# Performance work log

Measured on AMD Instinct MI355X. Metric: run time of the kernel, lower is better.

The kernel has to match this reference:

```python
import jax, jax.numpy as jnp
from jax import lax
import numpy as np

# dims
N_DIA, DLEN = 48, 64            # 48 dialogues, 64 utterances each
N = N_DIA * DLEN                # total utterances = 3072
D = 512                         # n_dim (modal feature dim)
H = 512                         # nhidden
NL = 2                          # GCNII layers
NS = 2                          # n_speakers
ALPHA, LAMDA = 0.1, 0.5
PI = float(np.pi)
SCALE = 0.99999                 # acos clamp factor from original code


def setup_inputs() -> dict:
    key = jax.random.key(0)
    ks = jax.random.split(key, 8)
    a = jax.random.normal(ks[0], (N, D), jnp.float32)
    v = jax.random.normal(ks[1], (N, D), jnp.float32)
    l = jax.random.normal(ks[2], (N, D), jnp.float32)
    qmask = jax.random.uniform(ks[3], (DLEN, N_DIA, NS), jnp.float32)
    dia_len = np.full((N_DIA,), DLEN, dtype=np.int64)  # static segment lengths
    # learned params
    W_spk = 0.02 * jax.random.normal(ks[4], (NS, D), jnp.float32)      # speaker_embeddings
    W0 = jax.random.normal(ks[5], (D, H), jnp.float32) / np.sqrt(D)    # graph_net.fcs[0]
    b0 = jnp.zeros((H,), jnp.float32)
    Wg = jax.random.normal(ks[6], (NL, H, H), jnp.float32) / np.sqrt(H)  # GCNII conv weights
    return {"a": a, "v": v, "l": l, "qmask": qmask, "dia_len": dia_len,
            "W_spk": W_spk, "W0": W0, "b0": b0, "Wg": Wg}


def _angular_sim(cs):
    # 1 - acos(cs*0.99999)/pi, clipped for numerical safety of acos
    return 1.0 - jnp.arccos(jnp.clip(cs * SCALE, -SCALE, SCALE)) / PI


def _build_adj(feats, seg_mask):
    # feats: list of 3 arrays [N, D]; seg_mask: [N, N] same-dialogue block mask
    n = feats[0].shape[0]
    normed = [f * jax.lax.rsqrt(jnp.sum(f * f, axis=1, keepdims=True)) for f in feats]
    adj = jnp.zeros((3 * n, 3 * n), feats[0].dtype)
    ar = jnp.arange(n)
    for m in range(3):
        for nn_ in range(3):
            if m == nn_:
                # within-modality: block-diagonal (per dialogue) angular cosine similarity
                sim = _angular_sim(normed[m] @ normed[m].T) * seg_mask
                adj = adj.at[m * n:(m + 1) * n, nn_ * n:(nn_ + 1) * n].set(sim)
            else:
                # cross-modality: only diagonal (same utterance) entries
                cs = jnp.sum(normed[m] * normed[nn_], axis=1)
                adj = adj.at[m * n + ar, nn_ * n + ar].set(_angular_sim(cs))
    # symmetric degree normalization D^-1/2 A D^-1/2
    dinv = jax.lax.rsqrt(adj.sum(axis=1))
    return adj * dinv[:, None] * dinv[None, :]


def reference(a, v, l, qmask, dia_len, W_spk, W0, b0, Wg):
    dl = np.asarray(dia_len)
    nb = dl.shape[0]
    # node -> (position-in-dialogue, dialogue-id), static from dia_len
    dia_id = np.repeat(np.arange(nb), dl)
    pos = np.concatenate([np.arange(x) for x in dl])
    qflat = qmask[pos, dia_id]                 # [N, NS], matches torch.cat order
    spk_idx = jnp.argmax(qflat, axis=-1)       # [N]
    l = l + W_spk[spk_idx]                     # use_speaker=True, 'l' in modals

    seg = jnp.asarray(dia_id)
    seg_mask = (seg[:, None] == seg[None, :]).astype(a.dtype)  # [N, N]
    adj = _build_adj([a, v, l], seg_mask)      # [3N, 3N]

    x = jnp.concatenate([a, v, l], axis=0)     # [3N, D]
    # GCNII_lyc (eval mode: dropout is identity)
    h0 = jax.nn.relu(x @ W0 + b0)              # [3N, H]
    thetas = jnp.log(LAMDA / jnp.arange(1, NL + 1, dtype=x.dtype) + 1.0)

    def step(h, wt):
        W, theta = wt
        hi = adj @ h
        support = (1.0 - ALPHA) * hi + ALPHA * h0   # variant=False
        h = jax.nn.relu(theta * (support @ W) + (1.0 - theta) * support)
        return h, None

    h, _ = lax.scan(step, h0, (Wg, thetas))
    feat = jnp.concatenate([x, h], axis=-1)    # use_residue=True -> [3N, D+H]
    n = a.shape[0]
    # regroup per-utterance modal features: [N, 3*(D+H)]
    out = jnp.concatenate([feat[:n], feat[n:2 * n], feat[2 * n:3 * n]], axis=-1)
    return out
```

## Files before the change

### kernel.cpp

```cpp
#include <hip/hip_runtime.h>
#include <math.h>

#define N_DIA 48
#define NTOT  3072
#define DD    512
#define M3    9216
#define SEG   ((size_t)NTOT * DD)

#define SCALE_F 0.99999f
#define PI_F    3.14159274101257324f

typedef __attribute__((ext_vector_type(8))) short frag8;
typedef __attribute__((ext_vector_type(4))) float f32x4;

__device__ __forceinline__ float ang_sim(float cs) {
    float cc = cs * SCALE_F;
    cc = fminf(fmaxf(cc, -SCALE_F), SCALE_F);
    return 1.0f - acosf(cc) / PI_F;
}
__device__ __forceinline__ unsigned short f2bf(float x) {
    union { float f; unsigned int u; } c; c.f = x;
    unsigned int r = c.u + 0x7fffu + ((c.u >> 16) & 1u);
    return (unsigned short)(r >> 16);
}
__device__ __forceinline__ float bf2f(unsigned short h) {
    union { unsigned int u; float f; } c; c.u = ((unsigned int)h) << 16;
    return c.f;
}
__device__ __forceinline__ void gload16(const unsigned short* g, unsigned short* s) {
    __builtin_amdgcn_global_load_lds(
        (const __attribute__((address_space(1))) unsigned int*)g,
        (__attribute__((address_space(3))) unsigned int*)s, 16, 0, 0);
}

__global__ __launch_bounds__(64) void k_pre(
    const float* __restrict__ a, const float* __restrict__ v,
    const float* __restrict__ l, const float* __restrict__ qmask,
    const float* __restrict__ Wspk,
    float* __restrict__ out, unsigned short* __restrict__ xb,
    float* __restrict__ invn, float* __restrict__ cross)
{
    int i = blockIdx.x, t = threadIdx.x;
    int pos = i & 63, dia = i >> 6;
    int qb = (pos * N_DIA + dia) * 2;
    float q0 = qmask[qb], q1 = qmask[qb + 1];
    int spk = (q0 >= q1) ? 0 : 1;
    const float4* av4 = (const float4*)(a + (size_t)i * DD);
    const float4* vv4 = (const float4*)(v + (size_t)i * DD);
    const float4* lv4 = (const float4*)(l + (size_t)i * DD);
    const float4* wv4 = (const float4*)(Wspk + (size_t)spk * DD);
    float* ob = out + (size_t)i * 3072;
    float saa = 0, svv = 0, sll = 0, sav = 0, sal = 0, svl = 0;
#pragma unroll
    for (int e = 0; e < 2; e++) {
        int idx = t * 2 + e;
        float4 xa = av4[idx], xv = vv4[idx], xd = lv4[idx], xw = wv4[idx];
        float4 xL = make_float4(xd.x + xw.x, xd.y + xw.y, xd.z + xw.z, xd.w + xw.w);
        *(float4*)(ob + idx * 4)        = xa;
        *(float4*)(ob + 1024 + idx * 4) = xv;
        *(float4*)(ob + 2048 + idx * 4) = xL;
        ushort4 ya, yv, yl;
        ya.x = f2bf(xa.x); ya.y = f2bf(xa.y); ya.z = f2bf(xa.z); ya.w = f2bf(xa.w);
        yv.x = f2bf(xv.x); yv.y = f2bf(xv.y); yv.z = f2bf(xv.z); yv.w = f2bf(xv.w);
        yl.x = f2bf(xL.x); yl.y = f2bf(xL.y); yl.z = f2bf(xL.z); yl.w = f2bf(xL.w);
        *(ushort4*)(xb + (size_t)i * DD + idx * 4) = ya;
        *(ushort4*)(xb + SEG + (size_t)i * DD + idx * 4) = yv;
        *(ushort4*)(xb + 2 * SEG + (size_t)i * DD + idx * 4) = yl;
        saa += xa.x * xa.x + xa.y * xa.y + xa.z * xa.z + xa.w * xa.w;
        svv += xv.x * xv.x + xv.y * xv.y + xv.z * xv.z + xv.w * xv.w;
        sll += xL.x * xL.x + xL.y * xL.y + xL.z * xL.z + xL.w * xL.w;
        sav += xa.x * xv.x + xa.y * xv.y + xa.z * xv.z + xa.w * xv.w;
        sal += xa.x * xL.x + xa.y * xL.y + xa.z * xL.z + xa.w * xL.w;
        svl += xv.x * xL.x + xv.y * xL.y + xv.z * xL.z + xv.w * xL.w;
    }
#pragma unroll
    for (int off = 32; off; off >>= 1) {
        saa += __shfl_down(saa, off, 64);
        svv += __shfl_down(svv, off, 64);
        sll += __shfl_down(sll, off, 64);
        sav += __shfl_down(sav, off, 64);
        sal += __shfl_down(sal, off, 64);
        svl += __shfl_down(svl, off, 64);
    }
    if (t == 0) {
        float ina = 1.0f / sqrtf(saa);
        float inv_ = 1.0f / sqrtf(svv);
        float inl = 1.0f / sqrtf(sll);
        invn[i] = ina; invn[NTOT + i] = inv_; invn[2 * NTOT + i] = inl;
        cross[i]            = ang_sim(sav * ina * inv_);
        cross[NTOT + i]     = ang_sim(sal * ina * inl);
        cross[2 * NTOT + i] = ang_sim(svl * inv_ * inl);
    }
}

__global__ __launch_bounds__(256) void k_gram_mfma(
    const unsigned short* __restrict__ xb, const float* __restrict__ invn,
    const float* __restrict__ cross, float* __restrict__ blk,
    float* __restrict__ dinv)
{
    __shared__ __align__(16) unsigned short Xs[16 * 2048];
    int d = blockIdx.x, m = blockIdx.y;
    int t = threadIdx.x;
    int lane = t & 63, wv = t >> 6;
    int mrow = m * NTOT + d * 64;
    const unsigned short* src = xb + (size_t)mrow * DD;
#pragma unroll
    for (int c = 0; c < 16; c++) {
        gload16(src + (size_t)(t >> 2) * DD + c * 32 + (t & 3) * 8,
                &Xs[c * 2048 + wv * 512]);
    }
    __syncthreads();

    int rsel = lane & 15, quad = lane >> 4;
    f32x4 acc[4];
#pragma unroll
    for (int j = 0; j < 4; j++) acc[j] = (f32x4){0.f, 0.f, 0.f, 0.f};
#pragma unroll
    for (int c = 0; c < 16; c++) {
        const unsigned short* base = &Xs[c * 2048];
        frag8 bf[4];
#pragma unroll
        for (int j = 0; j < 4; j++)
            bf[j] = *(const frag8*)&base[(j * 16 + rsel) * 32 + quad * 8];
        frag8 af = *(const frag8*)&base[(wv * 16 + rsel) * 32 + quad * 8];
#pragma unroll
        for (int j = 0; j < 4; j++)
            acc[j] = __builtin_amdgcn_mfma_f32_16x16x32_bf16(af, bf[j], acc[j], 0, 0, 0);
    }

    size_t bbase = (size_t)(m * N_DIA + d) * 4096;
    int rowl0 = wv * 16 + quad * 4;
    float ir[4], rs[4] = {0.f, 0.f, 0.f, 0.f};
#pragma unroll
    for (int r = 0; r < 4; r++) ir[r] = invn[mrow + rowl0 + r];
#pragma unroll
    for (int j = 0; j < 4; j++) {
        int coll = j * 16 + rsel;
        float ic = invn[mrow + coll];
#pragma unroll
        for (int r = 0; r < 4; r++) {
            float sim = ang_sim(acc[j][r] * ir[r] * ic);
            blk[bbase + (size_t)(rowl0 + r) * 64 + coll] = sim;
            rs[r] += sim;
        }
    }
#pragma unroll
    for (int off = 8; off; off >>= 1)
#pragma unroll
        for (int r = 0; r < 4; r++) rs[r] += __shfl_down(rs[r], off, 16);
    if (rsel == 0) {
#pragma unroll
        for (int r = 0; r < 4; r++) {
            int gi = d * 64 + rowl0 + r;
            float c1, c2;
            if (m == 0)      { c1 = cross[gi];        c2 = cross[NTOT + gi]; }
            else if (m == 1) { c1 = cross[gi];        c2 = cross[2 * NTOT + gi]; }
            else             { c1 = cross[NTOT + gi]; c2 = cross[2 * NTOT + gi]; }
            dinv[m * NTOT + gi] = 1.0f / sqrtf(rs[r] + c1 + c2);
        }
    }
}

__global__ void k_wt(const float* __restrict__ W0, const float* __restrict__ Wg,
                     unsigned short* __restrict__ Wt) {
    __shared__ float tile[32][33];
    int bx = blockIdx.x, by = blockIdx.y, mm = blockIdx.z;
    const float* W = (mm == 0) ? W0 : Wg + (size_t)(mm - 1) * DD * DD;
    int t = threadIdx.x;
    int tx = t & 31, ty = t >> 5;
#pragma unroll
    for (int q = 0; q < 4; q++) {
        int k = by * 32 + ty + q * 8;
        tile[ty + q * 8][tx] = W[(size_t)k * DD + bx * 32 + tx];
    }
    __syncthreads();
#pragma unroll
    for (int q = 0; q < 4; q++) {
        int n = bx * 32 + ty + q * 8;
        Wt[(size_t)mm * DD * DD + (size_t)n * DD + by * 32 + tx] = f2bf(tile[tx][ty + q * 8]);
    }
}

__global__ __launch_bounds__(256) void k_gemm_mfma(
    const unsigned short* __restrict__ A, const unsigned short* __restrict__ Wt,
    const float* __restrict__ bias, const unsigned short* __restrict__ resid,
    unsigned short* __restrict__ outT, unsigned short* __restrict__ outR,
    float* __restrict__ outF, float theta, int mode)
{
    __shared__ __align__(16) unsigned short As[64 * 32];
    __shared__ __align__(16) unsigned short Bs[128 * 32];
    int t = threadIdx.x;
    int lane = t & 63, wv = t >> 6;
    int mbase = blockIdx.y * 64, nbase = blockIdx.x * 128;
    int srow = lane >> 2;
    int scol = (lane & 3) * 8;
    int rsel = lane & 15, quad = lane >> 4;

    const unsigned short* Ag  = A  + (size_t)(mbase + wv * 16 + srow) * DD + scol;
    const unsigned short* Bg0 = Wt + (size_t)(nbase + wv * 32 + srow) * DD + scol;
    const unsigned short* Bg1 = Wt + (size_t)(nbase + wv * 32 + 16 + srow) * DD + scol;
    unsigned short* Asl  = &As[wv * 512];
    unsigned short* Bsl0 = &Bs[wv * 1024];
    unsigned short* Bsl1 = &Bs[wv * 1024 + 512];

    f32x4 acc[8];
#pragma unroll
    for (int i = 0; i < 8; i++) acc[i] = (f32x4){0.f, 0.f, 0.f, 0.f};

    for (int kt = 0; kt < DD; kt += 32) {
        __syncthreads();
        gload16(Ag + kt, Asl);
        gload16(Bg0 + kt, Bsl0);
        gload16(Bg1 + kt, Bsl1);
        __syncthreads();
        frag8 af[4], bfr[2];
#pragma unroll
        for (int i = 0; i < 4; i++)
            af[i] = *(const frag8*)&As[(i * 16 + rsel) * 32 + quad * 8];
#pragma unroll
        for (int j = 0; j < 2; j++)
            bfr[j] = *(const frag8*)&Bs[(wv * 32 + j * 16 + rsel) * 32 + quad * 8];
#pragma unroll
        for (int i = 0; i < 4; i++)
#pragma unroll
            for (int j = 0; j < 2; j++)
                acc[i * 2 + j] = __builtin_amdgcn_mfma_f32_16x16x32_bf16(
                    af[i], bfr[j], acc[i * 2 + j], 0, 0, 0);
    }

    float omt = 1.0f - theta;
    int mq = mbase / NTOT;
    int iu0 = mbase - mq * NTOT;
#pragma unroll
    for (int i = 0; i < 4; i++)
#pragma unroll
        for (int j = 0; j < 2; j++) {
            int col = nbase + wv * 32 + j * 16 + rsel;
            int rowl = i * 16 + quad * 4;
            int rowb = mbase + rowl;
            f32x4 r = acc[i * 2 + j];
            float vv[4];
#pragma unroll
            for (int rr = 0; rr < 4; rr++) {
                float x = r[rr];
                if (mode == 0) x += bias[col];
                else x = theta * x + omt * bf2f(resid[(size_t)(rowb + rr) * DD + col]);
                vv[rr] = fmaxf(x, 0.f);
            }
            if (mode == 2) {
#pragma unroll
                for (int rr = 0; rr < 4; rr++)
                    outF[(size_t)(iu0 + rowl + rr) * 3072 + mq * 1024 + 512 + col] = vv[rr];
            } else {
                ushort4 w4;
                w4.x = f2bf(vv[0]); w4.y = f2bf(vv[1]);
                w4.z = f2bf(vv[2]); w4.w = f2bf(vv[3]);
                *(ushort4*)(outT + (size_t)col * M3 + rowb) = w4;
#pragma unroll
                for (int rr = 0; rr < 4; rr++)
                    outR[(size_t)(rowb + rr) * DD + col] = f2bf(vv[rr]);
            }
        }
}

__global__ __launch_bounds__(256) void k_adjmul_mfma(
    const float* __restrict__ blk, const float* __restrict__ cross,
    const float* __restrict__ dinv,
    const unsigned short* __restrict__ hT, const unsigned short* __restrict__ hrow,
    const unsigned short* __restrict__ h0row, unsigned short* __restrict__ supb)
{
    __shared__ __align__(16) unsigned short AdL[64 * 72];
    __shared__ __align__(16) unsigned short hTL[256 * 72];
    __shared__ float dv[64];
    int cc = blockIdx.x, d = blockIdx.y, m = blockIdx.z;
    int t = threadIdx.x;
    int lane = t & 63, wv = t >> 6;
    int dbase = d * 64, cbase = cc * 256;
    int rsel = lane & 15, quad = lane >> 4;

    if (t < 64) dv[t] = dinv[m * NTOT + dbase + t];
    __syncthreads();

    size_t bbase = (size_t)(m * N_DIA + d) * 4096;
#pragma unroll
    for (int q = 0; q < 4; q++) {
        int e4 = t + 256 * q;
        int i = e4 >> 4, j4 = e4 & 15;
        float4 w = *(const float4*)(blk + bbase + (size_t)i * 64 + j4 * 4);
        float di = dv[i];
        ushort4 o;
        o.x = f2bf(w.x * di * dv[j4 * 4 + 0]);
        o.y = f2bf(w.y * di * dv[j4 * 4 + 1]);
        o.z = f2bf(w.z * di * dv[j4 * 4 + 2]);
        o.w = f2bf(w.w * di * dv[j4 * 4 + 3]);
        *(ushort4*)&AdL[i * 72 + j4 * 4] = o;
    }
#pragma unroll
    for (int p = 0; p < 8; p++) {
        int e = t + 256 * p;
        int cl = e >> 3;
        int jo = (e & 7) * 8;
        uint4 w = *(const uint4*)(hT + (size_t)(cbase + cl) * M3 + m * NTOT + dbase + jo);
        *(uint4*)&hTL[cl * 72 + jo] = w;
    }
    __syncthreads();

    f32x4 acc[16];
#pragma unroll
    for (int i = 0; i < 16; i++) acc[i] = (f32x4){0.f, 0.f, 0.f, 0.f};
#pragma unroll
    for (int kk = 0; kk < 2; kk++) {
        frag8 bfr[4];
#pragma unroll
        for (int it = 0; it < 4; it++)
            bfr[it] = *(const frag8*)&AdL[(it * 16 + rsel) * 72 + kk * 32 + quad * 8];
#pragma unroll
        for (int jc = 0; jc < 4; jc++) {
            frag8 af = *(const frag8*)&hTL[(wv * 64 + jc * 16 + rsel) * 72 + kk * 32 + quad * 8];
#pragma unroll
            for (int it = 0; it < 4; it++)
                acc[jc * 4 + it] = __builtin_amdgcn_mfma_f32_16x16x32_bf16(
                    af, bfr[it], acc[jc * 4 + it], 0, 0, 0);
        }
    }

    int n1, n2, p1, p2;
    if (m == 0)      { n1 = 1; n2 = 2; p1 = 0; p2 = 1; }
    else if (m == 1) { n1 = 0; n2 = 2; p1 = 0; p2 = 2; }
    else             { n1 = 0; n2 = 1; p1 = 1; p2 = 2; }
#pragma unroll
    for (int it = 0; it < 4; it++) {
        int il = it * 16 + rsel;
        int gi = dbase + il;
        float dm = dv[il];
        float cv1 = cross[p1 * NTOT + gi] * dm * dinv[n1 * NTOT + gi];
        float cv2 = cross[p2 * NTOT + gi] * dm * dinv[n2 * NTOT + gi];
        size_t r1 = (size_t)(n1 * NTOT + gi) * DD;
        size_t r2 = (size_t)(n2 * NTOT + gi) * DD;
        size_t r0 = (size_t)(m * NTOT + gi) * DD;
#pragma unroll
        for (int jc = 0; jc < 4; jc++) {
            int cb = cbase + wv * 64 + jc * 16 + quad * 4;
            ushort4 u1 = *(const ushort4*)(hrow + r1 + cb);
            ushort4 u2 = *(const ushort4*)(hrow + r2 + cb);
            ushort4 u0 = *(const ushort4*)(h0row + r0 + cb);
            f32x4 aa = acc[jc * 4 + it];
            ushort4 w;
            w.x = f2bf(0.9f * (aa[0] + cv1 * bf2f(u1.x) + cv2 * bf2f(u2.x)) + 0.1f * bf2f(u0.x));
            w.y = f2bf(0.9f * (aa[1] + cv1 * bf2f(u1.y) + cv2 * bf2f(u2.y)) + 0.1f * bf2f(u0.y));
            w.z = f2bf(0.9f * (aa[2] + cv1 * bf2f(u1.z) + cv2 * bf2f(u2.z)) + 0.1f * bf2f(u0.z));
            w.w = f2bf(0.9f * (aa[3] + cv1 * bf2f(u1.w) + cv2 * bf2f(u2.w)) + 0.1f * bf2f(u0.w));
            *(ushort4*)(supb + r0 + cb) = w;
        }
    }
}

extern "C" void kernel_launch(void* const* d_in, const int* in_sizes, int n_in,
                              void* d_out, int out_size, void* d_ws, size_t ws_size,
                              hipStream_t stream) {
    (void)in_sizes; (void)n_in; (void)out_size; (void)ws_size;
    const float* a     = (const float*)d_in[0];
    const float* v     = (const float*)d_in[1];
    const float* l     = (const float*)d_in[2];
    const float* qmask = (const float*)d_in[3];
    const float* Wspk  = (const float*)d_in[5];
    const float* W0    = (const float*)d_in[6];
    const float* b0    = (const float*)d_in[7];
    const float* Wg    = (const float*)d_in[8];
    float* out = (float*)d_out;
    float* ws = (float*)d_ws;

    float* invn  = ws;
    float* blk   = invn + M3;
    float* cross = blk + (size_t)3 * N_DIA * 4096;
    float* dinvp = cross + M3;
    unsigned short* Wt  = (unsigned short*)(dinvp + M3);
    unsigned short* xb  = Wt + (size_t)3 * DD * DD;
    unsigned short* supb = xb;
    unsigned short* h0T = xb + 3 * SEG;
    unsigned short* h0r = h0T + 3 * SEG;
    unsigned short* h1T = h0r + 3 * SEG;
    unsigned short* h1r = h1T + 3 * SEG;

    k_pre<<<NTOT, 64, 0, stream>>>(a, v, l, qmask, Wspk, out, xb, invn, cross);
    k_wt <<<dim3(16, 16, 3), 256, 0, stream>>>(W0, Wg, Wt);
    k_gram_mfma<<<dim3(N_DIA, 3), 256, 0, stream>>>(xb, invn, cross, blk, dinvp);

    const float th1 = 0.40546510810816438f;
    const float th2 = 0.22314355131420976f;

    k_gemm_mfma<<<dim3(4, 144), 256, 0, stream>>>(xb, Wt, b0, nullptr,
                                                  h0T, h0r, nullptr, 0.f, 0);
    k_adjmul_mfma<<<dim3(2, N_DIA, 3), 256, 0, stream>>>(blk, cross, dinvp,
                                                         h0T, h0r, h0r, supb);
    k_gemm_mfma<<<dim3(4, 144), 256, 0, stream>>>(supb, Wt + (size_t)DD * DD, nullptr, supb,
                                                  h1T, h1r, nullptr, th1, 1);
    k_adjmul_mfma<<<dim3(2, N_DIA, 3), 256, 0, stream>>>(blk, cross, dinvp,
                                                         h1T, h1r, h0r, supb);
    k_gemm_mfma<<<dim3(4, 144), 256, 0, stream>>>(supb, Wt + (size_t)2 * DD * DD, nullptr, supb,
                                                  nullptr, nullptr, out, th2, 2);
}
```

Measured before the change: 204.2 us.

## Reassociate GCNII layers to apply weights before adjacency, fuse prep kernels, swizzle LDS

Reorders each GCNII layer so the feature transform (theta*W + (1-theta)I) is applied before the adjacency multiply, which is valid because that map is linear. The adjacency kernel then emits the final ReLU output directly. This also removes a separate output GEMM pass, and the second layer's h0 transform is batched into the same GEMM launch. The prep and weight-transpose kernels are merged into one launch, and the GEMM gets double-buffered LDS loads with XOR-swizzled layouts. Outputs are staged through LDS for coalesced stores, and LDS bank conflicts are reduced in the gram and adjacency kernels. The reordering changes where bf16 rounding happens, which shifts numerics slightly.

```diff
diff --git a/kernel.cpp b/kernel.cpp
--- a/kernel.cpp
+++ b/kernel.cpp
@@ -33,63 +33,87 @@
         (__attribute__((address_space(3))) unsigned int*)s, 16, 0, 0);
 }
 
-__global__ __launch_bounds__(64) void k_pre(
+__global__ __launch_bounds__(256) void k_pre_wt(
     const float* __restrict__ a, const float* __restrict__ v,
     const float* __restrict__ l, const float* __restrict__ qmask,
-    const float* __restrict__ Wspk,
+    const float* __restrict__ Wspk, const float* __restrict__ W0,
+    const float* __restrict__ Wg,
     float* __restrict__ out, unsigned short* __restrict__ xb,
-    float* __restrict__ invn, float* __restrict__ cross)
+    float* __restrict__ invn, float* __restrict__ cross,
+    unsigned short* __restrict__ Wt)
 {
-    int i = blockIdx.x, t = threadIdx.x;
-    int pos = i & 63, dia = i >> 6;
-    int qb = (pos * N_DIA + dia) * 2;
-    float q0 = qmask[qb], q1 = qmask[qb + 1];
-    int spk = (q0 >= q1) ? 0 : 1;
-    const float4* av4 = (const float4*)(a + (size_t)i * DD);
-    const float4* vv4 = (const float4*)(v + (size_t)i * DD);
-    const float4* lv4 = (const float4*)(l + (size_t)i * DD);
-    const float4* wv4 = (const float4*)(Wspk + (size_t)spk * DD);
-    float* ob = out + (size_t)i * 3072;
-    float saa = 0, svv = 0, sll = 0, sav = 0, sal = 0, svl = 0;
-#pragma unroll
-    for (int e = 0; e < 2; e++) {
-        int idx = t * 2 + e;
-        float4 xa = av4[idx], xv = vv4[idx], xd = lv4[idx], xw = wv4[idx];
-        float4 xL = make_float4(xd.x + xw.x, xd.y + xw.y, xd.z + xw.z, xd.w + xw.w);
-        *(float4*)(ob + idx * 4)        = xa;
-        *(float4*)(ob + 1024 + idx * 4) = xv;
-        *(float4*)(ob + 2048 + idx * 4) = xL;
-        ushort4 ya, yv, yl;
-        ya.x = f2bf(xa.x); ya.y = f2bf(xa.y); ya.z = f2bf(xa.z); ya.w = f2bf(xa.w);
-        yv.x = f2bf(xv.x); yv.y = f2bf(xv.y); yv.z = f2bf(xv.z); yv.w = f2bf(xv.w);
-        yl.x = f2bf(xL.x); yl.y = f2bf(xL.y); yl.z = f2bf(xL.z); yl.w = f2bf(xL.w);
-        *(ushort4*)(xb + (size_t)i * DD + idx * 4) = ya;
-        *(ushort4*)(xb + SEG + (size_t)i * DD + idx * 4) = yv;
-        *(ushort4*)(xb + 2 * SEG + (size_t)i * DD + idx * 4) = yl;
-        saa += xa.x * xa.x + xa.y * xa.y + xa.z * xa.z + xa.w * xa.w;
-        svv += xv.x * xv.x + xv.y * xv.y + xv.z * xv.z + xv.w * xv.w;
-        sll += xL.x * xL.x + xL.y * xL.y + xL.z * xL.z + xL.w * xL.w;
-        sav += xa.x * xv.x + xa.y * xv.y + xa.z * xv.z + xa.w * xv.w;
-        sal += xa.x * xL.x + xa.y * xL.y + xa.z * xL.z + xa.w * xL.w;
-        svl += xv.x * xL.x + xv.y * xL.y + xv.z * xL.z + xv.w * xL.w;
-    }
-#pragma unroll
-    for (int off = 32; off; off >>= 1) {
-        saa += __shfl_down(saa, off, 64);
-        svv += __shfl_down(svv, off, 64);
-        sll += __shfl_down(sll, off, 64);
-        sav += __shfl_down(sav, off, 64);
-        sal += __shfl_down(sal, off, 64);
-        svl += __shfl_down(svl, off, 64);
-    }
-    if (t == 0) {
-        float ina = 1.0f / sqrtf(saa);
-        float inv_ = 1.0f / sqrtf(svv);
-        float inl = 1.0f / sqrtf(sll);
-        invn[i] = ina; invn[NTOT + i] = inv_; invn[2 * NTOT + i] = inl;
-        cross[i]            = ang_sim(sav * ina * inv_);
-        cross[NTOT + i]     = ang_sim(sal * ina * inl);
-        cross[2 * NTOT + i] = ang_sim(svl * inv_ * inl);
+    __shared__ float tile[32][33];
+    int b = blockIdx.x;
+    if (b < 768) {
+        int wv = threadIdx.x >> 6, t = threadIdx.x & 63;
+        int i = b * 4 + wv;
+        int pos = i & 63, dia = i >> 6;
+        int qb = (pos * N_DIA + dia) * 2;
+        float q0 = qmask[qb], q1 = qmask[qb + 1];
+        int spk = (q0 >= q1) ? 0 : 1;
+        const float4* av4 = (const float4*)(a + (size_t)i * DD);
+        const float4* vv4 = (const float4*)(v + (size_t)i * DD);
+        const float4* lv4 = (const float4*)(l + (size_t)i * DD);
+        const float4* wv4 = (const float4*)(Wspk + (size_t)spk * DD);
+        float* ob = out + (size_t)i * 3072;
+        float saa = 0, svv = 0, sll = 0, sav = 0, sal = 0, svl = 0;
+#pragma unroll
+        for (int e = 0; e < 2; e++) {
+            int idx = t * 2 + e;
+            float4 xa = av4[idx], xv = vv4[idx], xd = lv4[idx], xw = wv4[idx];
+            float4 xL = make_float4(xd.x + xw.x, xd.y + xw.y, xd.z + xw.z, xd.w + xw.w);
+            *(float4*)(ob + idx * 4)        = xa;
+            *(float4*)(ob + 1024 + idx * 4) = xv;
+            *(float4*)(ob + 2048 + idx * 4) = xL;
+            ushort4 ya, yv, yl;
+            ya.x = f2bf(xa.x); ya.y = f2bf(xa.y); ya.z = f2bf(xa.z); ya.w = f2bf(xa.w);
+            yv.x = f2bf(xv.x); yv.y = f2bf(xv.y); yv.z = f2bf(xv.z); yv.w = f2bf(xv.w);
+            yl.x = f2bf(xL.x); yl.y = f2bf(xL.y); yl.z = f2bf(xL.z); yl.w = f2bf(xL.w);
+            *(ushort4*)(xb + (size_t)i * DD + idx * 4) = ya;
+            *(ushort4*)(xb + SEG + (size_t)i * DD + idx * 4) = yv;
+            *(ushort4*)(xb + 2 * SEG + (size_t)i * DD + idx * 4) = yl;
+            saa += xa.x * xa.x + xa.y * xa.y + xa.z * xa.z + xa.w * xa.w;
+            svv += xv.x * xv.x + xv.y * xv.y + xv.z * xv.z + xv.w * xv.w;
+            sll += xL.x * xL.x + xL.y * xL.y + xL.z * xL.z + xL.w * xL.w;
+            sav += xa.x * xv.x + xa.y * xv.y + xa.z * xv.z + xa.w * xv.w;
+            sal += xa.x * xL.x + xa.y * xL.y + xa.z * xL.z + xa.w * xL.w;
+            svl += xv.x * xL.x + xv.y * xL.y + xv.z * xL.z + xv.w * xL.w;
+        }
+#pragma unroll
+        for (int off = 32; off; off >>= 1) {
+            saa += __shfl_down(saa, off, 64);
+            svv += __shfl_down(svv, off, 64);
+            sll += __shfl_down(sll, off, 64);
+            sav += __shfl_down(sav, off, 64);
+            sal += __shfl_down(sal, off, 64);
+            svl += __shfl_down(svl, off, 64);
+        }
+        if (t == 0) {
+            float ina = 1.0f / sqrtf(saa);
+            float inv_ = 1.0f / sqrtf(svv);
+            float inl = 1.0f / sqrtf(sll);
+            invn[i] = ina; invn[NTOT + i] = inv_; invn[2 * NTOT + i] = inl;
+            cross[i]            = ang_sim(sav * ina * inv_);
+            cross[NTOT + i]     = ang_sim(sal * ina * inl);
+            cross[2 * NTOT + i] = ang_sim(svl * inv_ * inl);
+        }
+    } else {
+        int idx = b - 768;
+        int mm = idx >> 8;
+        int by = (idx >> 4) & 15, bx = idx & 15;
+        const float* W = (mm == 0) ? W0 : Wg + (size_t)(mm - 1) * DD * DD;
+        int t = threadIdx.x, tx = t & 31, ty = t >> 5;
+#pragma unroll
+        for (int q = 0; q < 4; q++) {
+            int k = by * 32 + ty + q * 8;
+            tile[ty + q * 8][tx] = W[(size_t)k * DD + bx * 32 + tx];
+        }
+        __syncthreads();
+#pragma unroll
+        for (int q = 0; q < 4; q++) {
+            int n = bx * 32 + ty + q * 8;
+            Wt[(size_t)mm * DD * DD + (size_t)n * DD + by * 32 + tx] = f2bf(tile[tx][ty + q * 8]);
+        }
     }
 }
 
@@ -104,14 +128,16 @@
     int lane = t & 63, wv = t >> 6;
     int mrow = m * NTOT + d * 64;
     const unsigned short* src = xb + (size_t)mrow * DD;
+    int sunit = ((t & 3) ^ ((t >> 2) & 3)) * 8;
 #pragma unroll
     for (int c = 0; c < 16; c++) {
-        gload16(src + (size_t)(t >> 2) * DD + c * 32 + (t & 3) * 8,
+        gload16(src + (size_t)(t >> 2) * DD + c * 32 + sunit,
                 &Xs[c * 2048 + wv * 512]);
     }
     __syncthreads();
 
     int rsel = lane & 15, quad = lane >> 4;
+    int sq = (quad ^ (rsel & 3)) * 8;
     f32x4 acc[4];
 #pragma unroll
     for (int j = 0; j < 4; j++) acc[j] = (f32x4){0.f, 0.f, 0.f, 0.f};
@@ -121,8 +147,8 @@
         frag8 bf[4];
 #pragma unroll
         for (int j = 0; j < 4; j++)
-            bf[j] = *(const frag8*)&base[(j * 16 + rsel) * 32 + quad * 8];
-        frag8 af = *(const frag8*)&base[(wv * 16 + rsel) * 32 + quad * 8];
+            bf[j] = *(const frag8*)&base[(j * 16 + rsel) * 32 + sq];
+        frag8 af = *(const frag8*)&base[(wv * 16 + rsel) * 32 + sq];
 #pragma unroll
         for (int j = 0; j < 4; j++)
             acc[j] = __builtin_amdgcn_mfma_f32_16x16x32_bf16(af, bf[j], acc[j], 0, 0, 0);
@@ -161,65 +187,65 @@
     }
 }
 
-__global__ void k_wt(const float* __restrict__ W0, const float* __restrict__ Wg,
-                     unsigned short* __restrict__ Wt) {
-    __shared__ float tile[32][33];
-    int bx = blockIdx.x, by = blockIdx.y, mm = blockIdx.z;
-    const float* W = (mm == 0) ? W0 : Wg + (size_t)(mm - 1) * DD * DD;
-    int t = threadIdx.x;
-    int tx = t & 31, ty = t >> 5;
-#pragma unroll
-    for (int q = 0; q < 4; q++) {
-        int k = by * 32 + ty + q * 8;
-        tile[ty + q * 8][tx] = W[(size_t)k * DD + bx * 32 + tx];
-    }
-    __syncthreads();
-#pragma unroll
-    for (int q = 0; q < 4; q++) {
-        int n = bx * 32 + ty + q * 8;
-        Wt[(size_t)mm * DD * DD + (size_t)n * DD + by * 32 + tx] = f2bf(tile[tx][ty + q * 8]);
-    }
-}
-
-__global__ __launch_bounds__(256) void k_gemm_mfma(
-    const unsigned short* __restrict__ A, const unsigned short* __restrict__ Wt,
-    const float* __restrict__ bias, const unsigned short* __restrict__ resid,
-    unsigned short* __restrict__ outT, unsigned short* __restrict__ outR,
-    float* __restrict__ outF, float theta, int mode)
+__global__ __launch_bounds__(256) void k_gemm(
+    const unsigned short* __restrict__ A, const unsigned short* __restrict__ W,
+    const float* __restrict__ bias,
+    unsigned short* __restrict__ oRows, unsigned short* __restrict__ oT,
+    float theta, int mode,
+    const unsigned short* __restrict__ A2, unsigned short* __restrict__ oRows2)
 {
-    __shared__ __align__(16) unsigned short As[64 * 32];
-    __shared__ __align__(16) unsigned short Bs[128 * 32];
-    int t = threadIdx.x;
-    int lane = t & 63, wv = t >> 6;
-    int mbase = blockIdx.y * 64, nbase = blockIdx.x * 128;
+    __shared__ __align__(16) char smem[53248];
+    unsigned short* const As0 = (unsigned short*)smem;
+    unsigned short* const As1 = (unsigned short*)(smem + 4096);
+    unsigned short* const Bs0 = (unsigned short*)(smem + 8192);
+    unsigned short* const Bs1 = (unsigned short*)(smem + 16384);
+    unsigned short* const tH  = (unsigned short*)smem;
+    unsigned short* const tR  = (unsigned short*)(smem + 17408);
+    unsigned short* const tT  = (unsigned short*)(smem + 34816);
+
+    int t = threadIdx.x, lane = t & 63, wv = t >> 6;
+    int bx = blockIdx.x, by = blockIdx.y;
+    const unsigned short* Ap = A;
+    unsigned short* oR = oRows;
+    unsigned short* oTp = oT;
+    if (by >= 144) { Ap = A2; oR = oRows2; oTp = nullptr; by -= 144; }
+    int mbase = by * 64, nbase = bx * 128;
     int srow = lane >> 2;
-    int scol = (lane & 3) * 8;
+    int scol = (((lane & 3) ^ (srow & 3)) * 8);
     int rsel = lane & 15, quad = lane >> 4;
-
-    const unsigned short* Ag  = A  + (size_t)(mbase + wv * 16 + srow) * DD + scol;
-    const unsigned short* Bg0 = Wt + (size_t)(nbase + wv * 32 + srow) * DD + scol;
-    const unsigned short* Bg1 = Wt + (size_t)(nbase + wv * 32 + 16 + srow) * DD + scol;
-    unsigned short* Asl  = &As[wv * 512];
-    unsigned short* Bsl0 = &Bs[wv * 1024];
-    unsigned short* Bsl1 = &Bs[wv * 1024 + 512];
+    int sq = (quad ^ (rsel & 3)) * 8;
+
+    const unsigned short* Ag  = Ap + (size_t)(mbase + wv * 16 + srow) * DD + scol;
+    const unsigned short* Bg0 = W  + (size_t)(nbase + wv * 32 + srow) * DD + scol;
+    const unsigned short* Bg1 = W  + (size_t)(nbase + wv * 32 + 16 + srow) * DD + scol;
 
     f32x4 acc[8];
 #pragma unroll
     for (int i = 0; i < 8; i++) acc[i] = (f32x4){0.f, 0.f, 0.f, 0.f};
 
-    for (int kt = 0; kt < DD; kt += 32) {
+    gload16(Ag,  As0 + wv * 512);
+    gload16(Bg0, Bs0 + wv * 1024);
+    gload16(Bg1, Bs0 + wv * 1024 + 512);
+
+#pragma unroll
+    for (int kt = 0; kt < 16; kt++) {
         __syncthreads();
-        gload16(Ag + kt, Asl);
-        gload16(Bg0 + kt, Bsl0);
-        gload16(Bg1 + kt, Bsl1);
-        __syncthreads();
+        const unsigned short* Ac = (kt & 1) ? As1 : As0;
+        const unsigned short* Bc = (kt & 1) ? Bs1 : Bs0;
+        if (kt < 15) {
+            unsigned short* An = (kt & 1) ? As0 : As1;
+            unsigned short* Bn = (kt & 1) ? Bs0 : Bs1;
+            gload16(Ag + (kt + 1) * 32,  An + wv * 512);
+            gload16(Bg0 + (kt + 1) * 32, Bn + wv * 1024);
+            gload16(Bg1 + (kt + 1) * 32, Bn + wv * 1024 + 512);
+        }
         frag8 af[4], bfr[2];
 #pragma unroll
         for (int i = 0; i < 4; i++)
-            af[i] = *(const frag8*)&As[(i * 16 + rsel) * 32 + quad * 8];
+            af[i] = *(const frag8*)&Ac[(i * 16 + rsel) * 32 + sq];
 #pragma unroll
         for (int j = 0; j < 2; j++)
-            bfr[j] = *(const frag8*)&Bs[(wv * 32 + j * 16 + rsel) * 32 + quad * 8];
+            bfr[j] = *(const frag8*)&Bc[(wv * 32 + j * 16 + rsel) * 32 + sq];
 #pragma unroll
         for (int i = 0; i < 4; i++)
 #pragma unroll
@@ -227,55 +253,74 @@
                 acc[i * 2 + j] = __builtin_amdgcn_mfma_f32_16x16x32_bf16(
                     af[i], bfr[j], acc[i * 2 + j], 0, 0, 0);
     }
-
+    __syncthreads();
+
+    int r = t >> 2, c0 = (t & 3) * 32;
+    if (mode == 1) {
+        const unsigned short* srcA = Ap + (size_t)(mbase + r) * DD + nbase + c0;
+#pragma unroll
+        for (int u = 0; u < 4; u++)
+            *(uint4*)&tH[r * 136 + c0 + u * 8] = *(const uint4*)(srcA + u * 8);
+        __syncthreads();
+    }
     float omt = 1.0f - theta;
-    int mq = mbase / NTOT;
-    int iu0 = mbase - mq * NTOT;
 #pragma unroll
     for (int i = 0; i < 4; i++)
 #pragma unroll
         for (int j = 0; j < 2; j++) {
-            int col = nbase + wv * 32 + j * 16 + rsel;
-            int rowl = i * 16 + quad * 4;
-            int rowb = mbase + rowl;
-            f32x4 r = acc[i * 2 + j];
+            int cl = wv * 32 + j * 16 + rsel;
+            float bv = 0.f;
+            if (mode == 0) bv = bias[nbase + cl];
             float vv[4];
 #pragma unroll
             for (int rr = 0; rr < 4; rr++) {
-                float x = r[rr];
-                if (mode == 0) x += bias[col];
-                else x = theta * x + omt * bf2f(resid[(size_t)(rowb + rr) * DD + col]);
-                vv[rr] = fmaxf(x, 0.f);
+                int rl = i * 16 + quad * 4 + rr;
+                float x = acc[i * 2 + j][rr];
+                if (mode == 0) x = fmaxf(x + bv, 0.f);
+                else           x = theta * x + omt * bf2f(tH[rl * 136 + cl]);
+                vv[rr] = x;
             }
-            if (mode == 2) {
-#pragma unroll
-                for (int rr = 0; rr < 4; rr++)
-                    outF[(size_t)(iu0 + rowl + rr) * 3072 + mq * 1024 + 512 + col] = vv[rr];
-            } else {
+#pragma unroll
+            for (int rr = 0; rr < 4; rr++)
+                tR[(i * 16 + quad * 4 + rr) * 136 + cl] = f2bf(vv[rr]);
+            if (oTp) {
                 ushort4 w4;
                 w4.x = f2bf(vv[0]); w4.y = f2bf(vv[1]);
                 w4.z = f2bf(vv[2]); w4.w = f2bf(vv[3]);
-                *(ushort4*)(outT + (size_t)col * M3 + rowb) = w4;
-#pragma unroll
-                for (int rr = 0; rr < 4; rr++)
-                    outR[(size_t)(rowb + rr) * DD + col] = f2bf(vv[rr]);
+                *(ushort4*)&tT[cl * 72 + i * 16 + quad * 4] = w4;
             }
         }
-}
-
-__global__ __launch_bounds__(256) void k_adjmul_mfma(
+    __syncthreads();
+    {
+        unsigned short* dst = oR + (size_t)(mbase + r) * DD + nbase + c0;
+#pragma unroll
+        for (int u = 0; u < 4; u++)
+            *(uint4*)(dst + u * 8) = *(const uint4*)&tR[r * 136 + c0 + u * 8];
+    }
+    if (oTp) {
+        int c = t >> 1, r0 = (t & 1) * 32;
+        unsigned short* dst = oTp + (size_t)(nbase + c) * M3 + mbase + r0;
+#pragma unroll
+        for (int u = 0; u < 4; u++)
+            *(uint4*)(dst + u * 8) = *(const uint4*)&tT[c * 72 + r0 + u * 8];
+    }
+}
+
+__global__ __launch_bounds__(256) void k_adj(
     const float* __restrict__ blk, const float* __restrict__ cross,
     const float* __restrict__ dinv,
-    const unsigned short* __restrict__ hT, const unsigned short* __restrict__ hrow,
-    const unsigned short* __restrict__ h0row, unsigned short* __restrict__ supb)
+    const unsigned short* __restrict__ GT, const unsigned short* __restrict__ Gr,
+    const unsigned short* __restrict__ P0,
+    unsigned short* __restrict__ hout, float* __restrict__ outF, int final_mode)
 {
-    __shared__ __align__(16) unsigned short AdL[64 * 72];
-    __shared__ __align__(16) unsigned short hTL[256 * 72];
+    __shared__ __align__(16) unsigned short AdL[64 * 64];
+    __shared__ __align__(16) unsigned short GTL[256 * 64];
+    __shared__ __align__(16) unsigned short OT[64 * 264];
     __shared__ float dv[64];
-    int cc = blockIdx.x, d = blockIdx.y, m = blockIdx.z;
+    int ch = blockIdx.x, d = blockIdx.y, m = blockIdx.z;
     int t = threadIdx.x;
     int lane = t & 63, wv = t >> 6;
-    int dbase = d * 64, cbase = cc * 256;
+    int dbase = d * 64, cbase = ch * 256;
     int rsel = lane & 15, quad = lane >> 4;
 
     if (t < 64) dv[t] = dinv[m * NTOT + dbase + t];
@@ -293,15 +338,15 @@
         o.y = f2bf(w.y * di * dv[j4 * 4 + 1]);
         o.z = f2bf(w.z * di * dv[j4 * 4 + 2]);
         o.w = f2bf(w.w * di * dv[j4 * 4 + 3]);
-        *(ushort4*)&AdL[i * 72 + j4 * 4] = o;
+        *(ushort4*)((char*)AdL + i * 128 + (((j4 >> 1) ^ (i & 7)) << 4) + ((j4 & 1) << 3)) = o;
     }
 #pragma unroll
     for (int p = 0; p < 8; p++) {
         int e = t + 256 * p;
         int cl = e >> 3;
-        int jo = (e & 7) * 8;
-        uint4 w = *(const uint4*)(hT + (size_t)(cbase + cl) * M3 + m * NTOT + dbase + jo);
-        *(uint4*)&hTL[cl * 72 + jo] = w;
+        int uo = e & 7;
+        uint4 w = *(const uint4*)(GT + (size_t)(cbase + cl) * M3 + m * NTOT + dbase + uo * 8);
+        *(uint4*)((char*)GTL + cl * 128 + ((uo ^ (cl & 7)) << 4)) = w;
     }
     __syncthreads();
 
@@ -310,13 +355,14 @@
     for (int i = 0; i < 16; i++) acc[i] = (f32x4){0.f, 0.f, 0.f, 0.f};
 #pragma unroll
     for (int kk = 0; kk < 2; kk++) {
+        int su = ((kk * 4 + quad) ^ (rsel & 7)) << 4;
         frag8 bfr[4];
 #pragma unroll
         for (int it = 0; it < 4; it++)
-            bfr[it] = *(const frag8*)&AdL[(it * 16 + rsel) * 72 + kk * 32 + quad * 8];
+            bfr[it] = *(const frag8*)((const char*)AdL + (it * 16 + rsel) * 128 + su);
 #pragma unroll
         for (int jc = 0; jc < 4; jc++) {
-            frag8 af = *(const frag8*)&hTL[(wv * 64 + jc * 16 + rsel) * 72 + kk * 32 + quad * 8];
+            frag8 af = *(const frag8*)((const char*)GTL + (wv * 64 + jc * 16 + rsel) * 128 + su);
 #pragma unroll
             for (int it = 0; it < 4; it++)
                 acc[jc * 4 + it] = __builtin_amdgcn_mfma_f32_16x16x32_bf16(
@@ -340,18 +386,33 @@
         size_t r0 = (size_t)(m * NTOT + gi) * DD;
 #pragma unroll
         for (int jc = 0; jc < 4; jc++) {
-            int cb = cbase + wv * 64 + jc * 16 + quad * 4;
-            ushort4 u1 = *(const ushort4*)(hrow + r1 + cb);
-            ushort4 u2 = *(const ushort4*)(hrow + r2 + cb);
-            ushort4 u0 = *(const ushort4*)(h0row + r0 + cb);
+            int cl = wv * 64 + jc * 16 + quad * 4;
+            int cg = cbase + cl;
+            ushort4 u1 = *(const ushort4*)(Gr + r1 + cg);
+            ushort4 u2 = *(const ushort4*)(Gr + r2 + cg);
+            ushort4 u0 = *(const ushort4*)(P0 + r0 + cg);
             f32x4 aa = acc[jc * 4 + it];
-            ushort4 w;
-            w.x = f2bf(0.9f * (aa[0] + cv1 * bf2f(u1.x) + cv2 * bf2f(u2.x)) + 0.1f * bf2f(u0.x));
-            w.y = f2bf(0.9f * (aa[1] + cv1 * bf2f(u1.y) + cv2 * bf2f(u2.y)) + 0.1f * bf2f(u0.y));
-            w.z = f2bf(0.9f * (aa[2] + cv1 * bf2f(u1.z) + cv2 * bf2f(u2.z)) + 0.1f * bf2f(u0.z));
-            w.w = f2bf(0.9f * (aa[3] + cv1 * bf2f(u1.w) + cv2 * bf2f(u2.w)) + 0.1f * bf2f(u0.w));
-            *(ushort4*)(supb + r0 + cb) = w;
-        }
+            float o0 = fmaxf(0.9f * (aa[0] + cv1 * bf2f(u1.x) + cv2 * bf2f(u2.x)) + 0.1f * bf2f(u0.x), 0.f);
+            float o1 = fmaxf(0.9f * (aa[1] + cv1 * bf2f(u1.y) + cv2 * bf2f(u2.y)) + 0.1f * bf2f(u0.y), 0.f);
+            float o2 = fmaxf(0.9f * (aa[2] + cv1 * bf2f(u1.z) + cv2 * bf2f(u2.z)) + 0.1f * bf2f(u0.z), 0.f);
+            float o3 = fmaxf(0.9f * (aa[3] + cv1 * bf2f(u1.w) + cv2 * bf2f(u2.w)) + 0.1f * bf2f(u0.w), 0.f);
+            if (final_mode) {
+                *(float4*)(outF + (size_t)gi * 3072 + m * 1024 + 512 + cg) =
+                    make_float4(o0, o1, o2, o3);
+            } else {
+                ushort4 w;
+                w.x = f2bf(o0); w.y = f2bf(o1); w.z = f2bf(o2); w.w = f2bf(o3);
+                *(ushort4*)&OT[il * 264 + cl] = w;
+            }
+        }
+    }
+    if (!final_mode) {
+        __syncthreads();
+        int r = t >> 2, c0 = (t & 3) * 64;
+        unsigned short* dst = hout + (size_t)(m * NTOT + dbase + r) * DD + cbase + c0;
+#pragma unroll
+        for (int u = 0; u < 8; u++)
+            *(uint4*)(dst + u * 8) = *(const uint4*)&OT[r * 264 + c0 + u * 8];
     }
 }
 
@@ -376,27 +437,27 @@
     float* dinvp = cross + M3;
     unsigned short* Wt  = (unsigned short*)(dinvp + M3);
     unsigned short* xb  = Wt + (size_t)3 * DD * DD;
-    unsigned short* supb = xb;
-    unsigned short* h0T = xb + 3 * SEG;
-    unsigned short* h0r = h0T + 3 * SEG;
-    unsigned short* h1T = h0r + 3 * SEG;
-    unsigned short* h1r = h1T + 3 * SEG;
-
-    k_pre<<<NTOT, 64, 0, stream>>>(a, v, l, qmask, Wspk, out, xb, invn, cross);
-    k_wt <<<dim3(16, 16, 3), 256, 0, stream>>>(W0, Wg, Wt);
-    k_gram_mfma<<<dim3(N_DIA, 3), 256, 0, stream>>>(xb, invn, cross, blk, dinvp);
+    unsigned short* h0  = xb  + 3 * SEG;
+    unsigned short* G1r = h0  + 3 * SEG;
+    unsigned short* G1T = G1r + 3 * SEG;
+    unsigned short* h1  = G1T + 3 * SEG;
+    unsigned short* G2r = xb;
+    unsigned short* G2T = G1r;
+    unsigned short* P02 = G1T;
 
     const float th1 = 0.40546510810816438f;
     const float th2 = 0.22314355131420976f;
 
-    k_gemm_mfma<<<dim3(4, 144), 256, 0, stream>>>(xb, Wt, b0, nullptr,
-                                                  h0T, h0r, nullptr, 0.f, 0);
-    k_adjmul_mfma<<<dim3(2, N_DIA, 3), 256, 0, stream>>>(blk, cross, dinvp,
-                                                         h0T, h0r, h0r, supb);
-    k_gemm_mfma<<<dim3(4, 144), 256, 0, stream>>>(supb, Wt + (size_t)DD * DD, nullptr, supb,
-                                                  h1T, h1r, nullptr, th1, 1);
-    k_adjmul_mfma<<<dim3(2, N_DIA, 3), 256, 0, stream>>>(blk, cross, dinvp,
-                                                         h1T, h1r, h0r, supb);
-    k_gemm_mfma<<<dim3(4, 144), 256, 0, stream>>>(supb, Wt + (size_t)2 * DD * DD, nullptr, supb,
-                                                  nullptr, nullptr, out, th2, 2);
-}
+    k_pre_wt<<<1536, 256, 0, stream>>>(a, v, l, qmask, Wspk, W0, Wg, out, xb, invn, cross, Wt);
+    k_gram_mfma<<<dim3(N_DIA, 3), 256, 0, stream>>>(xb, invn, cross, blk, dinvp);
+
+    k_gemm<<<dim3(4, 144), 256, 0, stream>>>(xb, Wt, b0, h0, nullptr, 0.f, 0, nullptr, nullptr);
+    k_gemm<<<dim3(4, 144), 256, 0, stream>>>(h0, Wt + (size_t)DD * DD, nullptr, G1r, G1T,
+                                             th1, 1, nullptr, nullptr);
+    k_adj<<<dim3(2, N_DIA, 3), 256, 0, stream>>>(blk, cross, dinvp, G1T, G1r, G1r,
+                                                 h1, nullptr, 0);
+    k_gemm<<<dim3(4, 288), 256, 0, stream>>>(h1, Wt + (size_t)2 * DD * DD, nullptr, G2r, G2T,
+                                             th2, 1, h0, P02);
+    k_adj<<<dim3(2, N_DIA, 3), 256, 0, stream>>>(blk, cross, dinvp, G2T, G2r, P02,
+                                                 nullptr, out, 1);
+}
```

New measurement: 204.8 us. Within noise of the previous version (+0.3%).
